# Kernel optimization log

Hardware: AMD Instinct MI355X
Metric: run time of the kernel (lower is better)

## Reference

```python
import jax, jax.numpy as jnp
import numpy as np
from jax import lax

PATCH = 7
F_CH = 32      # args.F: adaConv output channels
N_FEATS = 64   # args.n_feats
F_HEAD = 64    # args.f
SCALE = 2
RGB_RANGE = 255.0
RGB_MEAN = jnp.array([0.4488, 0.4371, 0.4040], dtype=jnp.float32) * RGB_RANGE  # MeanShift, std=1


def _conv(x, w, b, padding):
    # x: NCHW, w: OIHW
    y = lax.conv_general_dilated(x, w, (1, 1), padding,
                                 dimension_numbers=('NCHW', 'OIHW', 'NCHW'))
    return y + b[None, :, None, None]


def _forward(x, w1, b1, w2, b2, wk, bk, wb, bb, w3, b3, w4, b4):
    B, C, H, W = x.shape
    x = x - RGB_MEAN[None, :, None, None]          # sub_mean
    # ---- Space2Batch(patch=7): pad to multiple of 7, patches -> batch dim ----
    pad_h = (-H) % PATCH
    pad_w = (-W) % PATCH
    xp = jnp.pad(x, ((0, 0), (0, 0), (0, pad_h), (0, pad_w)))
    Hp, Wp = H + pad_h, W + pad_w
    gh, gw = Hp // PATCH, Wp // PATCH
    patches = xp.reshape(B, C, gh, PATCH, gw, PATCH)
    patches = patches.transpose(0, 2, 4, 1, 3, 5).reshape(-1, C, PATCH, PATCH)  # (Bp,3,7,7)
    Bp = patches.shape[0]
    # ---- head: two valid 3x3 convs + ReLU -> (Bp, f, 3, 3) ----
    feat = jax.nn.relu(_conv(patches, w1, b1, 'VALID'))
    feat = jax.nn.relu(_conv(feat, w2, b2, 'VALID'))
    # ---- per-patch kernel / bias prediction (valid 3x3 -> 1x1 spatial) ----
    kern = _conv(feat, wk, bk, 'VALID').reshape(Bp, F_CH, 27)  # (F, Cin*kh*kw) per patch
    bias = _conv(feat, wb, bb, 'VALID').reshape(Bp, F_CH)
    # ---- adaConv: distinct predicted 3x3x3 kernel per patch, padding=1 ----
    xpad = jnp.pad(patches, ((0, 0), (0, 0), (1, 1), (1, 1)))
    # im2col ordered (C, kh, kw) to match torch kernel.view(-1, F, 3, 3, 3) flattening
    cols = jnp.stack([xpad[:, :, i:i + PATCH, j:j + PATCH]
                      for i in range(3) for j in range(3)], axis=2)  # (Bp, C, 9, 7, 7)
    cols = cols.reshape(Bp, C * 9, PATCH, PATCH)                    # (Bp, 27, 7, 7)
    y = jnp.einsum('bkhw,bfk->bfhw', cols, kern) + bias[:, :, None, None]  # (Bp, F, 7, 7)
    # ---- Batch2Space ----
    y = y.reshape(B, gh, gw, F_CH, PATCH, PATCH)
    y = y.transpose(0, 3, 1, 4, 2, 5).reshape(B, F_CH, Hp, Wp)
    # ---- body: conv5x5 F->n_feats + ReLU, conv3x3 n_feats -> 3*scale^2 ----
    y = jax.nn.relu(_conv(y, w3, b3, [(2, 2), (2, 2)]))
    y = _conv(y, w4, b4, [(1, 1), (1, 1)])
    # ---- PixelShuffle(scale) ----
    Bc, Cc, Hc, Wc = y.shape
    Co = Cc // (SCALE * SCALE)
    y = y.reshape(Bc, Co, SCALE, SCALE, Hc, Wc)
    y = y.transpose(0, 1, 4, 2, 5, 3).reshape(Bc, Co, Hc * SCALE, Wc * SCALE)
    y = y[..., :H * SCALE, :W * SCALE]
    return y + RGB_MEAN[None, :, None, None]       # add_mean


def setup_inputs() -> dict:
    key = jax.random.key(0)
    ks = jax.random.split(key, 8)

    def w(k, shape):
        fan_in = shape[1] * shape[2] * shape[3]
        return (jax.random.normal(k, shape, jnp.float32) / np.sqrt(fan_in)).astype(jnp.float32)

    f, Fc, n = F_HEAD, F_CH, N_FEATS
    return {
        'x': jax.random.uniform(ks[0], (4, 3, 360, 640), jnp.float32) * RGB_RANGE,
        'w1': w(ks[1], (f, 3, 3, 3)), 'b1': jnp.zeros((f,), jnp.float32),
        'w2': w(ks[2], (f, f, 3, 3)), 'b2': jnp.zeros((f,), jnp.float32),
        'wk': w(ks[3], (27 * Fc, f, 3, 3)), 'bk': jnp.zeros((27 * Fc,), jnp.float32),
        'wb': w(ks[4], (Fc, f, 3, 3)), 'bb': jnp.zeros((Fc,), jnp.float32),
        'w3': w(ks[5], (n, Fc, 5, 5)), 'b3': jnp.zeros((n,), jnp.float32),
        'w4': w(ks[6], (3 * SCALE * SCALE, n, 3, 3)), 'b4': jnp.zeros((3 * SCALE * SCALE,), jnp.float32),
    }


def reference(x, w1, b1, w2, b2, wk, bk, wb, bb, w3, b3, w4, b4):
    return _forward(x, w1, b1, w2, b2, wk, bk, wb, bb, w3, b3, w4, b4)
```

## Files before the change

kernel.cpp:

```cpp
#include <hip/hip_runtime.h>
#include <hip/hip_bf16.h>

#define GH 52
#define GW 92
#define BP 19136
#define HP 364
#define WP 644
#define HIN 360
#define WIN_ 640

#define Y32H 368
#define Y32W 648
#define Y64H 365
#define Y64W 645

typedef __attribute__((ext_vector_type(8))) short short8;
typedef __attribute__((ext_vector_type(4))) float f32x4;

__device__ __constant__ float c_mean[3] = {114.444f, 111.4605f, 103.02f};

#define OFF_FEAT1 0ULL
#define OFF_FEAT2 61235200ULL
#define OFF_KB2   83279872ULL
#define OFF_Y64P  0ULL
#define OFF_Y32P  122470400ULL
#define OFF_BMG   183517184ULL
#define OFF_W1T   183521280ULL
#define OFF_W2B   183528192ULL
#define OFF_WKB   183601920ULL
#define OFF_W3B   184781568ULL
#define OFF_W4B   184883968ULL
#define WS_NEED   184902400ULL

static __device__ __forceinline__ short bf16bits(float v) {
    __hip_bfloat16 h = __float2bfloat16(v);
    return *reinterpret_cast<short*>(&h);
}
static __device__ __forceinline__ float bits2f(short s) {
    __hip_bfloat16 h = *reinterpret_cast<__hip_bfloat16*>(&s);
    return __bfloat162float(h);
}

__global__ __launch_bounds__(256) void k_prep(
    const float* __restrict__ w1, float* __restrict__ w1t,
    const float* __restrict__ w2, short* __restrict__ w2b,
    const float* __restrict__ wk, const float* __restrict__ wb, short* __restrict__ wkb,
    const float* __restrict__ bk, const float* __restrict__ bb, float* __restrict__ bmg,
    const float* __restrict__ w3, short* __restrict__ w3b,
    const float* __restrict__ w4, short* __restrict__ w4b)
{
    int i = blockIdx.x * 256 + threadIdx.x;
    if (i < 1728) { int oc = i / 27, k = i % 27; w1t[k*64 + oc] = w1[i]; }
    if (i < 1024) {
        int f = i >> 5, k = i & 31;
        bmg[i] = (k < 27) ? bk[f*27 + k] : ((k == 27) ? bb[f] : 0.f);
    }
    if (i < 36864) {
        int c = i & 63; int rest = i >> 6; int oc = rest & 63; int tap = rest >> 6;
        int ky = tap / 3, kx = tap % 3;
        w2b[i] = bf16bits(w2[((oc*64 + c)*3 + ky)*3 + kx]);
    }
    if (i < 589824) {
        int n = i / 576, r = i % 576;
        int po = r >> 6, fch = r & 63;
        int ks = fch*9 + po;
        int f = n >> 5, k = n & 31;
        float v = 0.f;
        if (k < 27)       v = wk[(f*27 + k)*576 + ks];
        else if (k == 27) v = wb[f*576 + ks];
        wkb[i] = bf16bits(v);
    }
    if (i < 51200) {
        int c = i & 31; int rest = i >> 5; int oc = rest & 63; int tap = rest >> 6;
        int ky = tap / 5, kx = tap % 5;
        w3b[i] = bf16bits(w3[((oc*32 + c)*5 + ky)*5 + kx]);
    }
    if (i < 9216) {
        int c = i & 31; int rest = i >> 5; int n = rest & 15; rest >>= 4;
        int kh = rest & 1; int tap = rest >> 1;
        int ky = tap / 3, kx = tap % 3;
        float v = 0.f;
        if (n < 12) v = w4[((n*64 + kh*32 + c)*3 + ky)*3 + kx];
        w4b[i] = bf16bits(v);
    }
}

__global__ __launch_bounds__(256) void k_zg32(short* __restrict__ y32p)
{
    int u = blockIdx.x * 256 + threadIdx.x;
    if (u >= 64768) return;
    int b = u / 16192, r = u % 16192;
    int pxi = r >> 2, sub = r & 3;
    int row, col;
    if (pxi < 1296)      { row = pxi / 648;        col = pxi % 648; }
    else if (pxi < 2592) { row = 366 + (pxi-1296)/648; col = (pxi-1296) % 648; }
    else {
        int s = pxi - 2592;
        row = 2 + (s >> 2);
        int c4 = s & 3;
        col = (c4 < 2) ? c4 : (644 + c4);
    }
    uint4 z = make_uint4(0u,0u,0u,0u);
    *reinterpret_cast<uint4*>(y32p + (((size_t)b*Y32H + row)*Y32W + col)*32 + sub*8) = z;
}

__global__ __launch_bounds__(256) void k_zg64(short* __restrict__ y64p)
{
    int u = blockIdx.x * 256 + threadIdx.x;
    if (u >= 32288) return;
    int b = u / 8072, r = u % 8072;
    int pxi = r >> 3, sub = r & 7;
    int row, col;
    if (pxi < 645) { row = 0; col = pxi; }
    else           { row = pxi - 645 + 1; col = 0; }
    uint4 z = make_uint4(0u,0u,0u,0u);
    *reinterpret_cast<uint4*>(y64p + (((size_t)b*Y64H + row)*Y64W + col)*64 + sub*8) = z;
}

__global__ __launch_bounds__(256) void k_conv1(
    const float* __restrict__ x, const float* __restrict__ w1t, const float* __restrict__ b1,
    short* __restrict__ feat1)
{
    __shared__ float sp[16][148];
    const int tid = threadIdx.x;
    const int p0 = blockIdx.x * 16;

    for (int t = tid; t < 16*147; t += 256) {
        int p = t / 147, r = t % 147;
        int c = r / 49, rr = r % 49;
        int i = rr / 7, j = rr % 7;
        int pg = p0 + p;
        int b = pg / (GH*GW), rem = pg % (GH*GW);
        int gy = rem / GW, gx = rem % GW;
        int yy = gy*7 + i, xx = gx*7 + j;
        float v = 0.f;
        if (yy < HIN && xx < WIN_) v = x[((b*3 + c)*HIN + yy)*WIN_ + xx] - c_mean[c];
        sp[p][r] = v;
    }
    __syncthreads();

    for (int t = tid; t < 3200; t += 256) {
        int ocg = t & 7, p = (t >> 3) & 15, pos = t >> 7;
        int pi = pos / 5, pj = pos % 5;
        float acc[8];
        #pragma unroll
        for (int u = 0; u < 8; ++u) acc[u] = b1[ocg*8 + u];
        #pragma unroll
        for (int c = 0; c < 3; ++c)
            #pragma unroll
            for (int ki = 0; ki < 3; ++ki)
                #pragma unroll
                for (int kj = 0; kj < 3; ++kj) {
                    float fv = sp[p][c*49 + (pi+ki)*7 + (pj+kj)];
                    const float* wr = w1t + (c*9 + ki*3 + kj)*64 + ocg*8;
                    const float4 wa = *reinterpret_cast<const float4*>(wr);
                    const float4 wb4 = *reinterpret_cast<const float4*>(wr + 4);
                    acc[0] += fv*wa.x;  acc[1] += fv*wa.y;  acc[2] += fv*wa.z;  acc[3] += fv*wa.w;
                    acc[4] += fv*wb4.x; acc[5] += fv*wb4.y; acc[6] += fv*wb4.z; acc[7] += fv*wb4.w;
                }
        short8 pack;
        #pragma unroll
        for (int u = 0; u < 8; ++u) pack[u] = bf16bits(fmaxf(acc[u], 0.f));
        *reinterpret_cast<short8*>(feat1 + (size_t)pos*(BP*64) + (size_t)(p0 + p)*64 + ocg*8) = pack;
    }
}

__global__ __launch_bounds__(256) void k_conv2(
    const short* __restrict__ feat1, const short* __restrict__ w2b,
    const float* __restrict__ b2, short* __restrict__ feat2)
{
    const int tid = threadIdx.x;
    const int wv = tid >> 6, lane = tid & 63;
    const int n16 = lane & 15, q = lane >> 4;
    const int po = blockIdx.y;
    const int pi = po / 3, pj = po % 3;
    const int p0 = blockIdx.x * 128 + wv * 32;

    f32x4 acc[4][2];
    #pragma unroll
    for (int j = 0; j < 4; ++j) {
        float4 bj = *reinterpret_cast<const float4*>(b2 + j*16 + q*4);
        f32x4 bi = {bj.x, bj.y, bj.z, bj.w};
        acc[j][0] = bi; acc[j][1] = bi;
    }

    for (int ki = 0; ki < 3; ++ki)
        for (int kj = 0; kj < 3; ++kj) {
            const int tap = ki*3 + kj;
            const size_t base = (size_t)((pi+ki)*5 + (pj+kj)) * (BP*64);
            #pragma unroll
            for (int ks = 0; ks < 2; ++ks) {
                short8 af[4];
                #pragma unroll
                for (int j = 0; j < 4; ++j)
                    af[j] = *reinterpret_cast<const short8*>(w2b + (tap*64 + j*16 + n16)*64 + ks*32 + q*8);
                short8 bf[2];
                #pragma unroll
                for (int nt = 0; nt < 2; ++nt) {
                    int pr = p0 + nt*16 + n16; pr = (pr < BP) ? pr : (BP-1);
                    bf[nt] = *reinterpret_cast<const short8*>(feat1 + base + (size_t)pr*64 + ks*32 + q*8);
                }
                #pragma unroll
                for (int j = 0; j < 4; ++j)
                    #pragma unroll
                    for (int nt = 0; nt < 2; ++nt)
                        acc[j][nt] = __builtin_amdgcn_mfma_f32_16x16x32_bf16(af[j], bf[nt], acc[j][nt], 0, 0, 0);
            }
        }

    #pragma unroll
    for (int nt = 0; nt < 2; ++nt) {
        int pr = p0 + nt*16 + n16;
        if (pr >= BP) continue;
        #pragma unroll
        for (int j = 0; j < 4; ++j) {
            short4 pk;
            pk.x = bf16bits(fmaxf(acc[j][nt][0], 0.f));
            pk.y = bf16bits(fmaxf(acc[j][nt][1], 0.f));
            pk.z = bf16bits(fmaxf(acc[j][nt][2], 0.f));
            pk.w = bf16bits(fmaxf(acc[j][nt][3], 0.f));
            *reinterpret_cast<short4*>(feat2 + (size_t)po*(BP*64) + (size_t)pr*64 + j*16 + q*4) = pk;
        }
    }
}

__global__ __launch_bounds__(256) void k_gemm(
    const short* __restrict__ feat2, const short* __restrict__ wkb,
    const float* __restrict__ bmg, short* __restrict__ kb2)
{
    __shared__ __align__(16) short As[128*40];
    __shared__ __align__(16) short Bs[128*40];
    const int tid = threadIdx.x;
    const int p0 = blockIdx.x * 128, n0 = blockIdx.y * 128;
    const int wv = tid >> 6, lane = tid & 63;
    const int n16 = lane & 15, q = lane >> 4;
    const int wm = wv & 1, wn = wv >> 1;

    f32x4 acc[4][4] = {};

    for (int k0 = 0; k0 < 576; k0 += 32) {
        const int po = k0 >> 6, cb = k0 & 63;
        for (int t = tid; t < 512; t += 256) {
            int row = t >> 2, seg = t & 3;
            uint4 a = *reinterpret_cast<const uint4*>(wkb + (size_t)(n0 + row)*576 + k0 + seg*8);
            int pr = p0 + row; pr = (pr < BP) ? pr : (BP-1);
            uint4 b = *reinterpret_cast<const uint4*>(feat2 + (size_t)po*(BP*64) + (size_t)pr*64 + cb + seg*8);
            *reinterpret_cast<uint4*>(&As[row*40 + seg*8]) = a;
            *reinterpret_cast<uint4*>(&Bs[row*40 + seg*8]) = b;
        }
        __syncthreads();
        short8 af[4], bf[4];
        #pragma unroll
        for (int mt = 0; mt < 4; ++mt)
            af[mt] = *reinterpret_cast<const short8*>(&As[(wm*64 + mt*16 + n16)*40 + q*8]);
        #pragma unroll
        for (int nt = 0; nt < 4; ++nt)
            bf[nt] = *reinterpret_cast<const short8*>(&Bs[(wn*64 + nt*16 + n16)*40 + q*8]);
        #pragma unroll
        for (int mt = 0; mt < 4; ++mt)
            #pragma unroll
            for (int nt = 0; nt < 4; ++nt)
                acc[mt][nt] = __builtin_amdgcn_mfma_f32_16x16x32_bf16(af[mt], bf[nt], acc[mt][nt], 0, 0, 0);
        __syncthreads();
    }

    #pragma unroll
    for (int nt = 0; nt < 4; ++nt) {
        int pr = p0 + wn*64 + nt*16 + n16;
        if (pr >= BP) continue;
        #pragma unroll
        for (int mt = 0; mt < 4; ++mt) {
            int nb = n0 + wm*64 + mt*16 + q*4;
            float4 bs = *reinterpret_cast<const float4*>(bmg + nb);
            short4 pk;
            pk.x = bf16bits(acc[mt][nt][0] + bs.x);
            pk.y = bf16bits(acc[mt][nt][1] + bs.y);
            pk.z = bf16bits(acc[mt][nt][2] + bs.z);
            pk.w = bf16bits(acc[mt][nt][3] + bs.w);
            *reinterpret_cast<short4*>(kb2 + (size_t)pr*1024 + nb) = pk;
        }
    }
}

__global__ __launch_bounds__(256) void k_apply(
    const float* __restrict__ x, const short* __restrict__ kb2, short* __restrict__ y32p)
{
    __shared__ float pp[4][3][9][9];
    __shared__ __align__(16) short win[4*64*40];
    const int tid = threadIdx.x;
    const int wv = tid >> 6, lane = tid & 63;
    const int n16 = lane & 15, q = lane >> 4;
    const int p = blockIdx.x * 4 + wv;
    const int b = p / (GH*GW), rem = p % (GH*GW);
    const int gy = rem / GW, gx = rem % GW;
    const size_t kbase = (size_t)p * 1024;

    float* ppf = &pp[wv][0][0][0];
    for (int t = lane; t < 243; t += 64) ppf[t] = 0.f;
    {
        uint4 z = make_uint4(0u,0u,0u,0u);
        uint4* wr = reinterpret_cast<uint4*>(&win[(wv*64 + lane)*40]);
        #pragma unroll
        for (int u = 0; u < 5; ++u) wr[u] = z;
    }
    for (int t = lane; t < 147; t += 64) {
        int c = t / 49, r = t % 49, i = r / 7, j = r % 7;
        int yy = gy*7 + i, xx = gx*7 + j;
        float v = 0.f;
        if (yy < HIN && xx < WIN_) v = x[((b*3 + c)*HIN + yy)*WIN_ + xx] - c_mean[c];
        pp[wv][c][i+1][j+1] = v;
    }
    if (lane < 49) {
        int h = lane / 7, w = lane % 7;
        short* dst = &win[(wv*64 + lane)*40];
        #pragma unroll
        for (int c = 0; c < 3; ++c)
            #pragma unroll
            for (int i = 0; i < 3; ++i)
                #pragma unroll
                for (int j = 0; j < 3; ++j)
                    dst[c*9 + i*3 + j] = bf16bits(pp[wv][c][h+i][w+j]);
    }

    short8 af0 = *reinterpret_cast<const short8*>(kb2 + kbase + (size_t)(n16)*32 + q*8);
    short8 af1 = *reinterpret_cast<const short8*>(kb2 + kbase + (size_t)(16 + n16)*32 + q*8);

    f32x4 acc[2][4];
    #pragma unroll
    for (int mt = 0; mt < 2; ++mt) {
        f32x4 bi;
        #pragma unroll
        for (int r = 0; r < 4; ++r) bi[r] = bits2f(kb2[kbase + (size_t)(mt*16 + q*4 + r)*32 + 27]);
        #pragma unroll
        for (int nt = 0; nt < 4; ++nt) acc[mt][nt] = bi;
    }
    #pragma unroll
    for (int nt = 0; nt < 4; ++nt) {
        short8 bf = *reinterpret_cast<const short8*>(&win[(wv*64 + nt*16 + n16)*40 + q*8]);
        acc[0][nt] = __builtin_amdgcn_mfma_f32_16x16x32_bf16(af0, bf, acc[0][nt], 0, 0, 0);
        acc[1][nt] = __builtin_amdgcn_mfma_f32_16x16x32_bf16(af1, bf, acc[1][nt], 0, 0, 0);
    }

    #pragma unroll
    for (int nt = 0; nt < 4; ++nt) {
        int px = nt*16 + n16;
        if (px < 49) {
            int h = px / 7, w = px % 7;
            short* dst = y32p + (((size_t)b*Y32H + gy*7 + h + 2)*Y32W + gx*7 + w + 2)*32;
            #pragma unroll
            for (int mt = 0; mt < 2; ++mt) {
                short4 pk;
                pk.x = bf16bits(acc[mt][nt][0]);
                pk.y = bf16bits(acc[mt][nt][1]);
                pk.z = bf16bits(acc[mt][nt][2]);
                pk.w = bf16bits(acc[mt][nt][3]);
                *reinterpret_cast<short4*>(dst + mt*16 + q*4) = pk;
            }
        }
    }
}

__global__ __launch_bounds__(256, 2) void k_conv3(
    const short* __restrict__ y32p, const short* __restrict__ w3b,
    const float* __restrict__ b3, short* __restrict__ y64p)
{
    __shared__ __align__(16) short sin_[20*40*40];
    const int tid = threadIdx.x;
    const int wv = tid >> 6, lane = tid & 63;
    const int n16 = lane & 15, q = lane >> 4;
    const int x0 = blockIdx.x * 32, y0 = blockIdx.y * 16, b = blockIdx.z;

    for (int t = tid; t < 2880; t += 256) {
        int pix = t >> 2, q4 = t & 3;
        int row = pix / 36, col = pix % 36;
        int ry = y0 + row; ry = (ry < Y32H) ? ry : (Y32H - 1);
        int cx = x0 + col; cx = (cx < Y32W) ? cx : (Y32W - 1);
        uint4 v = *reinterpret_cast<const uint4*>(
            y32p + (((size_t)b*Y32H + ry)*Y32W + cx)*32 + q4*8);
        *reinterpret_cast<uint4*>(&sin_[(row*40 + col)*40 + q4*8]) = v;
    }
    __syncthreads();

    f32x4 acc[4][2][4];
    #pragma unroll
    for (int j = 0; j < 4; ++j) {
        float4 bj = *reinterpret_cast<const float4*>(b3 + j*16 + q*4);
        f32x4 bi = {bj.x, bj.y, bj.z, bj.w};
        #pragma unroll
        for (int i = 0; i < 4; ++i) {
            acc[i][0][j] = bi; acc[i][1][j] = bi;
        }
    }

    for (int ky = 0; ky < 5; ++ky) {
        for (int kx = 0; kx < 5; ++kx) {
            const int tap = ky*5 + kx;
            short8 afw[4];
            #pragma unroll
            for (int j = 0; j < 4; ++j)
                afw[j] = *reinterpret_cast<const short8*>(w3b + (tap*64 + j*16 + n16)*32 + q*8);
            short8 bfa[4][2];
            #pragma unroll
            for (int i = 0; i < 4; ++i)
                #pragma unroll
                for (int g = 0; g < 2; ++g) {
                    int pixslot = (wv*4 + i + ky)*40 + (g*16 + n16 + kx);
                    bfa[i][g] = *reinterpret_cast<const short8*>(&sin_[pixslot*40 + q*8]);
                }
            #pragma unroll
            for (int i = 0; i < 4; ++i)
                #pragma unroll
                for (int g = 0; g < 2; ++g)
                    #pragma unroll
                    for (int j = 0; j < 4; ++j)
                        acc[i][g][j] = __builtin_amdgcn_mfma_f32_16x16x32_bf16(afw[j], bfa[i][g], acc[i][g][j], 0, 0, 0);
        }
    }

    #pragma unroll
    for (int g = 0; g < 2; ++g) {
        int ox = x0 + g*16 + n16;
        if (ox >= WP) continue;
        #pragma unroll
        for (int i = 0; i < 4; ++i) {
            int oy = y0 + wv*4 + i;
            if (oy >= HP) continue;
            short* dst = y64p + (((size_t)b*Y64H + oy + 1)*Y64W + ox + 1)*64;
            #pragma unroll
            for (int j = 0; j < 4; ++j) {
                short4 pk;
                pk.x = bf16bits(fmaxf(acc[i][g][j][0], 0.f));
                pk.y = bf16bits(fmaxf(acc[i][g][j][1], 0.f));
                pk.z = bf16bits(fmaxf(acc[i][g][j][2], 0.f));
                pk.w = bf16bits(fmaxf(acc[i][g][j][3], 0.f));
                *reinterpret_cast<short4*>(dst + j*16 + q*4) = pk;
            }
        }
    }
}

__global__ __launch_bounds__(256) void k_conv4(
    const short* __restrict__ y64p, const short* __restrict__ w4b,
    const float* __restrict__ b4, float* __restrict__ out)
{
    __shared__ __align__(16) short sin_[18*18*72];
    const int tid = threadIdx.x;
    const int wv = tid >> 6, lane = tid & 63;
    const int n16 = lane & 15, q = lane >> 4;
    const int x0 = blockIdx.x * 16, y0 = blockIdx.y * 16, b = blockIdx.z;

    for (int t = tid; t < 2592; t += 256) {
        int pix = t >> 3, sub = t & 7;
        int row = pix / 18, col = pix % 18;
        int ry = y0 + row; ry = (ry < Y64H) ? ry : (Y64H - 1);
        int cx = x0 + col;
        uint4 v = *reinterpret_cast<const uint4*>(
            y64p + (((size_t)b*Y64H + ry)*Y64W + cx)*64 + sub*8);
        *reinterpret_cast<uint4*>(&sin_[pix*72 + sub*8]) = v;
    }
    __syncthreads();

    f32x4 acc[4];
    {
        f32x4 bi = {0.f, 0.f, 0.f, 0.f};
        if (q < 3) {
            float4 bq = *reinterpret_cast<const float4*>(b4 + q*4);
            bi = {bq.x, bq.y, bq.z, bq.w};
        }
        #pragma unroll
        for (int i = 0; i < 4; ++i) acc[i] = bi;
    }

    for (int ky = 0; ky < 3; ++ky) {
        #pragma unroll
        for (int kx = 0; kx < 3; ++kx) {
            const int tap = ky*3 + kx;
            short8 af0 = *reinterpret_cast<const short8*>(w4b + ((tap*2 + 0)*16 + n16)*32 + q*8);
            short8 af1 = *reinterpret_cast<const short8*>(w4b + ((tap*2 + 1)*16 + n16)*32 + q*8);
            #pragma unroll
            for (int i = 0; i < 4; ++i) {
                int pix = (wv*4 + i + ky)*18 + (n16 + kx);
                short8 a0 = *reinterpret_cast<const short8*>(&sin_[pix*72 + q*8]);
                short8 a1 = *reinterpret_cast<const short8*>(&sin_[pix*72 + 32 + q*8]);
                acc[i] = __builtin_amdgcn_mfma_f32_16x16x32_bf16(af0, a0, acc[i], 0, 0, 0);
                acc[i] = __builtin_amdgcn_mfma_f32_16x16x32_bf16(af1, a1, acc[i], 0, 0, 0);
            }
        }
    }

    if (q < 3) {
        const int xx = x0 + n16;
        const float m = c_mean[q];
        #pragma unroll
        for (int i = 0; i < 4; ++i) {
            int yy = y0 + wv*4 + i;
            if (yy >= HIN) continue;
            size_t r0 = ((size_t)(b*3 + q)*720 + yy*2)*1280 + xx*2;
            float2 s0 = {acc[i][0] + m, acc[i][1] + m};
            float2 s1 = {acc[i][2] + m, acc[i][3] + m};
            *reinterpret_cast<float2*>(out + r0) = s0;
            *reinterpret_cast<float2*>(out + r0 + 1280) = s1;
        }
    }
}

extern "C" void kernel_launch(void* const* d_in, const int* in_sizes, int n_in,
                              void* d_out, int out_size, void* d_ws, size_t ws_size,
                              hipStream_t stream) {
    const float* x  = (const float*)d_in[0];
    const float* w1 = (const float*)d_in[1];
    const float* b1 = (const float*)d_in[2];
    const float* w2 = (const float*)d_in[3];
    const float* b2 = (const float*)d_in[4];
    const float* wk = (const float*)d_in[5];
    const float* bk = (const float*)d_in[6];
    const float* wb = (const float*)d_in[7];
    const float* bb = (const float*)d_in[8];
    const float* w3 = (const float*)d_in[9];
    const float* b3 = (const float*)d_in[10];
    const float* w4 = (const float*)d_in[11];
    const float* b4 = (const float*)d_in[12];
    float* out = (float*)d_out;

    if (ws_size < WS_NEED) return;

    char* ws = (char*)d_ws;
    short* feat1 = (short*)(ws + OFF_FEAT1);
    short* feat2 = (short*)(ws + OFF_FEAT2);
    short* kb2   = (short*)(ws + OFF_KB2);
    short* y32p  = (short*)(ws + OFF_Y32P);
    short* y64p  = (short*)(ws + OFF_Y64P);
    float* bmg = (float*)(ws + OFF_BMG);
    float* w1t = (float*)(ws + OFF_W1T);
    short* w2b = (short*)(ws + OFF_W2B);
    short* wkb = (short*)(ws + OFF_WKB);
    short* w3b = (short*)(ws + OFF_W3B);
    short* w4b = (short*)(ws + OFF_W4B);

    k_prep <<<2304, 256, 0, stream>>>(w1, w1t, w2, w2b, wk, wb, wkb, bk, bb, bmg, w3, w3b, w4, w4b);
    k_zg32 <<<254, 256, 0, stream>>>(y32p);
    k_conv1<<<BP/16, 256, 0, stream>>>(x, w1t, b1, feat1);
    k_conv2<<<dim3(150, 9), 256, 0, stream>>>(feat1, w2b, b2, feat2);
    k_gemm <<<dim3(150, 8), 256, 0, stream>>>(feat2, wkb, bmg, kb2);
    k_apply<<<BP/4, 256, 0, stream>>>(x, kb2, y32p);
    k_zg64 <<<127, 256, 0, stream>>>(y64p);
    k_conv3<<<dim3(21, 23, 4), 256, 0, stream>>>(y32p, w3b, b3, y64p);
    k_conv4<<<dim3(40, 23, 4), 256, 0, stream>>>(y64p, w4b, b4, out);
}
```

Measured before the change: 456.1 us.

## Swizzle LDS tiles in conv kernels and fold adaConv bias into MFMA

The conv3 and conv4 shared-memory tiles drop their padded strides (40/72 shorts) for dense strides (32/64) with an XOR swizzle on the 16-byte chunk index. This keeps ds_read bank conflicts low while shrinking LDS use, so launch bounds are raised to allow three blocks per CU. The adaConv kernel now places a constant 1.0 in im2col slot 27, so the predicted bias is applied by the MFMA itself and the scalar bias loads are removed. The higher occupancy target may force register spills in conv3, whose accumulators are large.

```diff
diff --git a/kernel.cpp b/kernel.cpp
--- a/kernel.cpp
+++ b/kernel.cpp
@@ -302,6 +302,7 @@
         uint4* wr = reinterpret_cast<uint4*>(&win[(wv*64 + lane)*40]);
         #pragma unroll
         for (int u = 0; u < 5; ++u) wr[u] = z;
+        win[(wv*64 + lane)*40 + 27] = (short)0x3F80;
     }
     for (int t = lane; t < 147; t += 64) {
         int c = t / 49, r = t % 49, i = r / 7, j = r % 7;
@@ -325,15 +326,7 @@
     short8 af0 = *reinterpret_cast<const short8*>(kb2 + kbase + (size_t)(n16)*32 + q*8);
     short8 af1 = *reinterpret_cast<const short8*>(kb2 + kbase + (size_t)(16 + n16)*32 + q*8);
 
-    f32x4 acc[2][4];
-    #pragma unroll
-    for (int mt = 0; mt < 2; ++mt) {
-        f32x4 bi;
-        #pragma unroll
-        for (int r = 0; r < 4; ++r) bi[r] = bits2f(kb2[kbase + (size_t)(mt*16 + q*4 + r)*32 + 27]);
-        #pragma unroll
-        for (int nt = 0; nt < 4; ++nt) acc[mt][nt] = bi;
-    }
+    f32x4 acc[2][4] = {};
     #pragma unroll
     for (int nt = 0; nt < 4; ++nt) {
         short8 bf = *reinterpret_cast<const short8*>(&win[(wv*64 + nt*16 + n16)*40 + q*8]);
@@ -360,11 +353,11 @@
     }
 }
 
-__global__ __launch_bounds__(256, 2) void k_conv3(
+__global__ __launch_bounds__(256, 3) void k_conv3(
     const short* __restrict__ y32p, const short* __restrict__ w3b,
     const float* __restrict__ b3, short* __restrict__ y64p)
 {
-    __shared__ __align__(16) short sin_[20*40*40];
+    __shared__ __align__(16) short sin_[20*36*32];
     const int tid = threadIdx.x;
     const int wv = tid >> 6, lane = tid & 63;
     const int n16 = lane & 15, q = lane >> 4;
@@ -377,7 +370,7 @@
         int cx = x0 + col; cx = (cx < Y32W) ? cx : (Y32W - 1);
         uint4 v = *reinterpret_cast<const uint4*>(
             y32p + (((size_t)b*Y32H + ry)*Y32W + cx)*32 + q4*8);
-        *reinterpret_cast<uint4*>(&sin_[(row*40 + col)*40 + q4*8]) = v;
+        *reinterpret_cast<uint4*>(&sin_[pix*32 + ((q4 ^ ((col >> 1) & 3))*8)]) = v;
     }
     __syncthreads();
 
@@ -399,13 +392,19 @@
             #pragma unroll
             for (int j = 0; j < 4; ++j)
                 afw[j] = *reinterpret_cast<const short8*>(w3b + (tap*64 + j*16 + n16)*32 + q*8);
+            int swg[2], colg[2];
+            #pragma unroll
+            for (int g = 0; g < 2; ++g) {
+                colg[g] = g*16 + n16 + kx;
+                swg[g] = (q ^ ((colg[g] >> 1) & 3)) * 8;
+            }
             short8 bfa[4][2];
             #pragma unroll
             for (int i = 0; i < 4; ++i)
                 #pragma unroll
                 for (int g = 0; g < 2; ++g) {
-                    int pixslot = (wv*4 + i + ky)*40 + (g*16 + n16 + kx);
-                    bfa[i][g] = *reinterpret_cast<const short8*>(&sin_[pixslot*40 + q*8]);
+                    int pix = (wv*4 + i + ky)*36 + colg[g];
+                    bfa[i][g] = *reinterpret_cast<const short8*>(&sin_[pix*32 + swg[g]]);
                 }
             #pragma unroll
             for (int i = 0; i < 4; ++i)
@@ -439,11 +438,11 @@
     }
 }
 
-__global__ __launch_bounds__(256) void k_conv4(
+__global__ __launch_bounds__(256, 3) void k_conv4(
     const short* __restrict__ y64p, const short* __restrict__ w4b,
     const float* __restrict__ b4, float* __restrict__ out)
 {
-    __shared__ __align__(16) short sin_[18*18*72];
+    __shared__ __align__(16) short sin_[18*18*64];
     const int tid = threadIdx.x;
     const int wv = tid >> 6, lane = tid & 63;
     const int n16 = lane & 15, q = lane >> 4;
@@ -456,7 +455,7 @@
         int cx = x0 + col;
         uint4 v = *reinterpret_cast<const uint4*>(
             y64p + (((size_t)b*Y64H + ry)*Y64W + cx)*64 + sub*8);
-        *reinterpret_cast<uint4*>(&sin_[pix*72 + sub*8]) = v;
+        *reinterpret_cast<uint4*>(&sin_[pix*64 + ((sub ^ ((col >> 1) & 7))*8)]) = v;
     }
     __syncthreads();
 
@@ -477,11 +476,14 @@
             const int tap = ky*3 + kx;
             short8 af0 = *reinterpret_cast<const short8*>(w4b + ((tap*2 + 0)*16 + n16)*32 + q*8);
             short8 af1 = *reinterpret_cast<const short8*>(w4b + ((tap*2 + 1)*16 + n16)*32 + q*8);
+            const int col = n16 + kx;
+            const int s0 = (q ^ ((col >> 1) & 7)) * 8;
+            const int s1 = ((q + 4) ^ ((col >> 1) & 7)) * 8;
             #pragma unroll
             for (int i = 0; i < 4; ++i) {
-                int pix = (wv*4 + i + ky)*18 + (n16 + kx);
-                short8 a0 = *reinterpret_cast<const short8*>(&sin_[pix*72 + q*8]);
-                short8 a1 = *reinterpret_cast<const short8*>(&sin_[pix*72 + 32 + q*8]);
+                int pix = (wv*4 + i + ky)*18 + col;
+                short8 a0 = *reinterpret_cast<const short8*>(&sin_[pix*64 + s0]);
+                short8 a1 = *reinterpret_cast<const short8*>(&sin_[pix*64 + s1]);
                 acc[i] = __builtin_amdgcn_mfma_f32_16x16x32_bf16(af0, a0, acc[i], 0, 0, 0);
                 acc[i] = __builtin_amdgcn_mfma_f32_16x16x32_bf16(af1, a1, acc[i], 0, 0, 0);
             }
```

Result: slower. 761.6 us (+67.0%).
